# Performance work log

Hardware: AMD Instinct MI355X
Metric: run time of the kernel (lower is better)

The kernel has to match this reference:

```python
import jax, jax.numpy as jnp
import numpy as np

N, D, H, DATT, C, NCLS = 20000, 1024, 512, 256, 10, 4

def setup_inputs() -> dict:
    key = jax.random.key(0)
    ks = jax.random.split(key, 20)
    s = lambda fan_in: 1.0 / np.sqrt(fan_in)
    u = lambda k, shape, fan_in: jax.random.uniform(k, shape, jnp.float32, -s(fan_in), s(fan_in))
    inp = {
        'x': jax.random.normal(ks[0], (N, D), jnp.float32),
        'cluster_id': jax.random.randint(ks[1], (N,), 0, C),
        # per-cluster expert MLP (phi_i): Linear(D,H)+ReLU, Linear(H,H)+ReLU (dropout=identity in eval)
        'W1': u(ks[2], (C, D, H), D), 'b1': u(ks[3], (C, H), D),
        'W2': u(ks[4], (C, H, H), H), 'b2': u(ks[5], (C, H), H),
        # attention_net: Linear(H,H)+ReLU then gated attention (L=H, D=DATT, n_classes=1)
        'fc_W': u(ks[6], (H, H), H), 'fc_b': u(ks[7], (H,), H),
        'Wa': u(ks[8], (H, DATT), H), 'ba': u(ks[9], (DATT,), H),
        'Wb': u(ks[10], (H, DATT), H), 'bb': u(ks[11], (DATT,), H),
        'Wc': u(ks[12], (DATT, 1), DATT), 'bc': u(ks[13], (1,), DATT),
        # rho: Linear(H, DATT)+ReLU
        'rho_W': u(ks[14], (H, DATT), H), 'rho_b': u(ks[15], (DATT,), H),
        # classifier
        'cls_W': u(ks[16], (DATT, NCLS), DATT), 'cls_b': u(ks[17], (NCLS,), DATT),
    }
    return inp

def reference(x, cluster_id, W1, b1, W2, b2, fc_W, fc_b, Wa, ba, Wb, bb, Wc, bc, rho_W, rho_b, cls_W, cls_b):
    # --- per-cluster expert MLPs, vectorized over clusters (no python loop over data) ---
    # h1: [C, N, H] = ReLU(x @ W1_c + b1_c) for every cluster c
    h1 = jax.nn.relu(jnp.einsum('nd,cdh->cnh', x, W1) + b1[:, None, :])
    h2 = jax.nn.relu(jnp.einsum('cnh,chk->cnk', h1, W2) + b2[:, None, :])
    # masked mean-pool per cluster (AdaptiveAvgPool1d(1) over the cluster's tokens)
    mask = (cluster_id[None, :] == jnp.arange(C)[:, None]).astype(h2.dtype)  # [C, N]
    counts = jnp.maximum(mask.sum(axis=1), 1.0)                               # empty cluster -> zeros
    h_cluster = jnp.einsum('cn,cnh->ch', mask, h2) / counts[:, None]          # [C, H]
    # --- attention net: fc + gated attention ---
    h = jax.nn.relu(h_cluster @ fc_W + fc_b)                                  # [C, H]
    a = jnp.tanh(h @ Wa + ba)
    b = jax.nn.sigmoid(h @ Wb + bb)
    A = ((a * b) @ Wc + bc).T                                                 # [1, C]
    A = jax.nn.softmax(A, axis=1)
    h_path = A @ h                                                            # [1, H]
    hr = jax.nn.relu(h_path @ rho_W + rho_b)[0]                               # [DATT] (squeeze)
    logits = (hr @ cls_W + cls_b)[None, :]                                    # [1, NCLS]
    Y_prob = jax.nn.softmax(logits, axis=1)
    Y_hat = jnp.argmax(logits, axis=1, keepdims=True)
    return (logits, Y_prob, Y_hat)
```

## Files before the change

### kernel.cpp

```cpp
#include <hip/hip_runtime.h>
#include <hip/hip_bf16.h>
#include <stdint.h>

#define NT 20000
#define DIM 1024
#define HID 512
#define DATT_N 256
#define NCLUS 10
#define NCLS_N 4
#define NBS 79
#define NRT2 313

typedef __bf16 bf16;
typedef __attribute__((ext_vector_type(8))) __bf16 bf16x8;
typedef __attribute__((ext_vector_type(4))) float f32x4;

__device__ __forceinline__ void gload_lds16(const void* g, void* l) {
  __builtin_amdgcn_global_load_lds(
      (const __attribute__((address_space(1))) unsigned int*)g,
      (__attribute__((address_space(3))) unsigned int*)l, 16, 0, 0);
}


__device__ __forceinline__ void transpose_body(const float* __restrict__ s,
                                               bf16* __restrict__ d, int R, int Cc,
                                               int i0, int j0, float (*t)[33]) {
  int tx = threadIdx.x & 31, ty = threadIdx.x >> 5;
#pragma unroll
  for (int yy = 0; yy < 32; yy += 8)
    t[ty + yy][tx] = s[(size_t)(i0 + ty + yy) * Cc + (j0 + tx)];
  __syncthreads();
#pragma unroll
  for (int yy = 0; yy < 32; yy += 8)
    d[(size_t)(j0 + ty + yy) * R + (i0 + tx)] = (bf16)t[tx][ty + yy];
}

#define ZPB ((NCLUS * HID + 255) / 256)
#define TW1B (16 * 32 * NCLUS)
#define TW2B (16 * 16 * NCLUS)

__global__ __launch_bounds__(256) void setup_kernel(
    const int* __restrict__ cid, int* __restrict__ blkcnt, float* __restrict__ pool,
    const float* __restrict__ W1, bf16* __restrict__ w1t,
    const float* __restrict__ W2, bf16* __restrict__ w2t) {
  __shared__ float t[32][33];
  __shared__ int wcnt[4][16];
  int b = blockIdx.x;
  int tid = threadIdx.x;
  if (b < NBS) {
    int lane = tid & 63, w = tid >> 6;
    int n = b * 256 + tid;
    int mycid = (n < NT) ? cid[n] : -1;
#pragma unroll
    for (int c = 0; c < NCLUS; ++c) {
      unsigned long long m = __ballot(mycid == c);
      if (lane == c) wcnt[w][c] = __popcll(m);
    }
    __syncthreads();
    if (tid < NCLUS)
      blkcnt[b * NCLUS + tid] =
          wcnt[0][tid] + wcnt[1][tid] + wcnt[2][tid] + wcnt[3][tid];
  } else if (b < NBS + ZPB) {
    int i = (b - NBS) * 256 + tid;
    if (i < NCLUS * HID) pool[i] = 0.f;
  } else if (b < NBS + ZPB + TW1B) {
    int bb = b - NBS - ZPB;
    int z = bb >> 9, r = bb & 511, y = r >> 4, x = r & 15;
    transpose_body(W1 + (size_t)z * DIM * HID, w1t + (size_t)z * DIM * HID,
                   DIM, HID, y * 32, x * 32, t);
  } else {
    int bb = b - NBS - ZPB - TW1B;
    int z = bb >> 8, r = bb & 255, y = r >> 4, x = r & 15;
    transpose_body(W2 + (size_t)z * HID * HID, w2t + (size_t)z * HID * HID,
                   HID, HID, y * 32, x * 32, t);
  }
}

__global__ void prefix_kernel(const int* __restrict__ blkcnt, int* __restrict__ blkbase,
                              int* __restrict__ cnt, int* __restrict__ offs) {
  int c = threadIdx.x;
  if (c < NCLUS) {
    int run = 0;
    for (int b = 0; b < NBS; ++b) {
      blkbase[b * NCLUS + c] = run;
      run += blkcnt[b * NCLUS + c];
    }
    cnt[c] = run;
  }
  __syncthreads();
  if (c == 0) {
    int a = 0;
    for (int i = 0; i < NCLUS; ++i) { offs[i] = a; a += cnt[i]; }
    offs[NCLUS] = a;
  }
}

__global__ __launch_bounds__(256) void scatter2_kernel(
    const int* __restrict__ cid, const int* __restrict__ blkbase,
    const int* __restrict__ offs, int* __restrict__ order) {
  __shared__ int wcnt[4][16];
  __shared__ int wbase[4][16];
  int tid = threadIdx.x;
  int lane = tid & 63, w = tid >> 6;
  int n = blockIdx.x * 256 + tid;
  int mycid = (n < NT) ? cid[n] : -1;
  unsigned long long lmask = (lane == 63) ? ~0ull >> 1 : (1ull << lane) - 1;
  int myrank = 0;
#pragma unroll
  for (int c = 0; c < NCLUS; ++c) {
    unsigned long long m = __ballot(mycid == c);
    if (mycid == c) myrank = __popcll(m & lmask);
    if (lane == c) wcnt[w][c] = __popcll(m);
  }
  __syncthreads();
  if (tid < NCLUS) {
    int pre = blkbase[blockIdx.x * NCLUS + tid];
#pragma unroll
    for (int ww = 0; ww < 4; ++ww) { wbase[ww][tid] = pre; pre += wcnt[ww][tid]; }
  }
  __syncthreads();
  if (n < NT) order[offs[mycid] + wbase[w][mycid] + myrank] = n;
}

__global__ void gather_cast(const float* __restrict__ x, const int* __restrict__ order,
                            bf16* __restrict__ xs) {
  int t = blockIdx.x * 256 + threadIdx.x;
  int row = t >> 7;
  if (row >= NT) return;
  int col = (t & 127) << 3;
  const f32x4* p = (const f32x4*)(x + (size_t)order[row] * DIM + col);
  f32x4 u = p[0], v = p[1];
  bf16x8 w;
  w[0] = (bf16)u[0]; w[1] = (bf16)u[1]; w[2] = (bf16)u[2]; w[3] = (bf16)u[3];
  w[4] = (bf16)v[0]; w[5] = (bf16)v[1]; w[6] = (bf16)v[2]; w[7] = (bf16)v[3];
  *(bf16x8*)(xs + (size_t)row * DIM + col) = w;
}

__device__ __forceinline__ bool decode_grp2(int d, int& c, int& rt, int& j) {
  int x8 = d & 7, s = d >> 3;
  int g = (s >> 2) * 8 + x8;
  if (g >= NRT2 * NCLUS) return false;
  j = s & 3;
  c = g / NRT2;
  rt = g - c * NRT2;
  return true;
}


__global__ __launch_bounds__(128, 3) void gemm1_kernel(
    const bf16* __restrict__ xs, const bf16* __restrict__ w1t, const float* __restrict__ b1,
    const int* __restrict__ offs, const int* __restrict__ cnt, bf16* __restrict__ h1) {
  int c, rt, j;
  if (!decode_grp2(blockIdx.x, c, rt, j)) return;
  int cntc = cnt[c];
  int row0 = rt * 64;
  if (row0 >= cntc) return;
  int seg = offs[c];
  int n0 = j * 128;

  __shared__ bf16 Als[64 * 64];
  __shared__ bf16 Bls[128 * 64];

  int tid = threadIdx.x;
  int lane = tid & 63, w = tid >> 6;
  int rx = lane & 7, hi = lane >> 4;

  int kswz = ((lane & 7) ^ (lane >> 3)) << 3;

  const bf16* aptr[4]; int aoff[4];
  const bf16* bptr[8]; int boff[8];
#pragma unroll
  for (int i = 0; i < 4; ++i) {
    int ch = i * 2 + w;
    int r = ch * 8 + (lane >> 3);
    int ar = seg + row0 + r; if (ar > NT - 1) ar = NT - 1;
    aptr[i] = xs + (size_t)ar * DIM + kswz;
    aoff[i] = ch * 512;
  }
#pragma unroll
  for (int i = 0; i < 8; ++i) {
    int ch = i * 2 + w;
    int r = ch * 8 + (lane >> 3);
    bptr[i] = w1t + (size_t)(c * HID + n0 + r) * DIM + kswz;
    boff[i] = ch * 512;
  }

  f32x4 acc[2][8];
#pragma unroll
  for (int m = 0; m < 2; m++)
#pragma unroll
    for (int n = 0; n < 8; n++) acc[m][n] = {0.f, 0.f, 0.f, 0.f};

  for (int k0 = 0; k0 < DIM; k0 += 64) {
#pragma unroll
    for (int i = 0; i < 4; ++i) gload_lds16(aptr[i] + k0, &Als[aoff[i]]);
#pragma unroll
    for (int i = 0; i < 8; ++i) gload_lds16(bptr[i] + k0, &Bls[boff[i]]);
    __syncthreads();
#pragma unroll
    for (int ks = 0; ks < 2; ++ks) {
      int t16 = ks * 4 + hi;
      int ko = ((t16 ^ rx) << 3);
      bf16x8 a[2], b[8];
#pragma unroll
      for (int m = 0; m < 2; m++)
        a[m] = *(const bf16x8*)(&Als[(w * 32 + m * 16 + (lane & 15)) * 64 + ko]);
#pragma unroll
      for (int n = 0; n < 8; n++)
        b[n] = *(const bf16x8*)(&Bls[(n * 16 + (lane & 15)) * 64 + ko]);
#pragma unroll
      for (int m = 0; m < 2; m++)
#pragma unroll
        for (int n = 0; n < 8; n++)
          acc[m][n] = __builtin_amdgcn_mfma_f32_16x16x32_bf16(a[m], b[n], acc[m][n], 0, 0, 0);
    }
    __syncthreads();
  }

  int valid = cntc - row0; if (valid > 64) valid = 64;
#pragma unroll
  for (int n = 0; n < 8; n++) {
    int col = n0 + n * 16 + (lane & 15);
    float bias = b1[c * HID + col];
#pragma unroll
    for (int m = 0; m < 2; m++) {
      int rbase = w * 32 + m * 16 + ((lane >> 4) << 2);
#pragma unroll
      for (int e = 0; e < 4; e++) {
        int r = rbase + e;
        if (r < valid) {
          float v = acc[m][n][e] + bias;
          h1[(size_t)(seg + row0 + r) * HID + col] = (bf16)(v > 0.f ? v : 0.f);
        }
      }
    }
  }
}


__global__ __launch_bounds__(128, 3) void gemm2_kernel(
    const bf16* __restrict__ h1, const bf16* __restrict__ w2t, const float* __restrict__ b2,
    const int* __restrict__ offs, const int* __restrict__ cnt, float* __restrict__ pool) {
  int c, rt, j;
  if (!decode_grp2(blockIdx.x, c, rt, j)) return;
  int cntc = cnt[c];
  int row0 = rt * 64;
  if (row0 >= cntc) return;
  int seg = offs[c];
  int n0 = j * 128;
  int valid = cntc - row0; if (valid > 64) valid = 64;

  __shared__ bf16 Als[64 * 64];
  __shared__ bf16 Bls[128 * 64];

  int tid = threadIdx.x;
  int lane = tid & 63, w = tid >> 6;
  int rx = lane & 7, hi = lane >> 4;
  int kswz = ((lane & 7) ^ (lane >> 3)) << 3;

  const bf16* aptr[4]; int aoff[4];
  const bf16* bptr[8]; int boff[8];
#pragma unroll
  for (int i = 0; i < 4; ++i) {
    int ch = i * 2 + w;
    int r = ch * 8 + (lane >> 3);
    int ar = seg + row0 + r; if (ar > NT - 1) ar = NT - 1;
    aptr[i] = h1 + (size_t)ar * HID + kswz;
    aoff[i] = ch * 512;
  }
#pragma unroll
  for (int i = 0; i < 8; ++i) {
    int ch = i * 2 + w;
    int r = ch * 8 + (lane >> 3);
    bptr[i] = w2t + (size_t)(c * HID + n0 + r) * HID + kswz;
    boff[i] = ch * 512;
  }

  f32x4 acc[2][8];
#pragma unroll
  for (int m = 0; m < 2; m++)
#pragma unroll
    for (int n = 0; n < 8; n++) acc[m][n] = {0.f, 0.f, 0.f, 0.f};

  for (int k0 = 0; k0 < HID; k0 += 64) {
#pragma unroll
    for (int i = 0; i < 4; ++i) gload_lds16(aptr[i] + k0, &Als[aoff[i]]);
#pragma unroll
    for (int i = 0; i < 8; ++i) gload_lds16(bptr[i] + k0, &Bls[boff[i]]);
    __syncthreads();
#pragma unroll
    for (int ks = 0; ks < 2; ++ks) {
      int t16 = ks * 4 + hi;
      int ko = ((t16 ^ rx) << 3);
      bf16x8 a[2], b[8];
#pragma unroll
      for (int m = 0; m < 2; m++)
        a[m] = *(const bf16x8*)(&Als[(w * 32 + m * 16 + (lane & 15)) * 64 + ko]);
#pragma unroll
      for (int n = 0; n < 8; n++)
        b[n] = *(const bf16x8*)(&Bls[(n * 16 + (lane & 15)) * 64 + ko]);
#pragma unroll
      for (int m = 0; m < 2; m++)
#pragma unroll
        for (int n = 0; n < 8; n++)
          acc[m][n] = __builtin_amdgcn_mfma_f32_16x16x32_bf16(a[m], b[n], acc[m][n], 0, 0, 0);
    }
    __syncthreads();
  }

#pragma unroll
  for (int n = 0; n < 8; n++) {
    int col = n0 + n * 16 + (lane & 15);
    float bias = b2[c * HID + col];
    float s = 0.f;
#pragma unroll
    for (int m = 0; m < 2; m++) {
      int rbase = w * 32 + m * 16 + ((lane >> 4) << 2);
#pragma unroll
      for (int e = 0; e < 4; e++) {
        if (rbase + e < valid) {
          float v = acc[m][n][e] + bias;
          s += (v > 0.f ? v : 0.f);
        }
      }
    }
    s += __shfl_xor(s, 16);
    s += __shfl_xor(s, 32);
    if (lane < 16) atomicAdd(&pool[c * HID + col], s);
  }
}


__global__ __launch_bounds__(256) void tail_fc(
    const float* __restrict__ pool, const int* __restrict__ cnt,
    const float* __restrict__ fcW, const float* __restrict__ fcb,
    float* __restrict__ hbuf) {
  int c = blockIdx.x >> 3;
  int jt = blockIdx.x & 7;
  __shared__ float hc[HID];
  __shared__ float red[4][64];
  int tid = threadIdx.x;
  float inv = 1.f / fmaxf((float)cnt[c], 1.f);
  for (int k = tid; k < HID; k += 256) hc[k] = pool[c * HID + k] * inv;
  __syncthreads();
  int jl = tid & 63, kg = tid >> 6;
  int j = jt * 64 + jl;
  float s = 0.f;
#pragma unroll 4
  for (int k = kg * 128; k < kg * 128 + 128; ++k) s += hc[k] * fcW[(size_t)k * HID + j];
  red[kg][jl] = s;
  __syncthreads();
  if (kg == 0) {
    float v = red[0][jl] + red[1][jl] + red[2][jl] + red[3][jl] + fcb[j];
    hbuf[c * HID + j] = fmaxf(v, 0.f);
  }
}

__global__ __launch_bounds__(1024) void tail_att(
    const float* __restrict__ hbuf,
    const float* __restrict__ Wa, const float* __restrict__ ba,
    const float* __restrict__ Wb, const float* __restrict__ bb,
    const float* __restrict__ Wc, const float* __restrict__ bc,
    float* __restrict__ score) {
  int c = blockIdx.x;
  __shared__ float h[HID];
  __shared__ float ra[4][DATT_N];
  __shared__ float rb[4][DATT_N];
  __shared__ float sc[DATT_N];
  int tid = threadIdx.x;
  for (int k = tid; k < HID; k += 1024) h[k] = hbuf[c * HID + k];
  __syncthreads();
  int jl = tid & 255, kg = tid >> 8;
  float sa = 0.f, sb = 0.f;
#pragma unroll 4
  for (int k = kg * 128; k < kg * 128 + 128; ++k) {
    float hv = h[k];
    sa += hv * Wa[(size_t)k * DATT_N + jl];
    sb += hv * Wb[(size_t)k * DATT_N + jl];
  }
  ra[kg][jl] = sa;
  rb[kg][jl] = sb;
  __syncthreads();
  if (kg == 0) {
    float va = ra[0][jl] + ra[1][jl] + ra[2][jl] + ra[3][jl] + ba[jl];
    float vb = rb[0][jl] + rb[1][jl] + rb[2][jl] + rb[3][jl] + bb[jl];
    float av = tanhf(va);
    float bv = 1.f / (1.f + expf(-vb));
    sc[jl] = av * bv * Wc[jl];
  }
  __syncthreads();
  for (int s2 = 128; s2 > 0; s2 >>= 1) {
    if (tid < s2) sc[tid] += sc[tid + s2];
    __syncthreads();
  }
  if (tid == 0) score[c] = sc[0] + bc[0];
}

__global__ __launch_bounds__(1024) void tail_fin(
    const float* __restrict__ score, const float* __restrict__ hbuf,
    const float* __restrict__ rhoW, const float* __restrict__ rhob,
    const float* __restrict__ clsW, const float* __restrict__ clsb,
    float* __restrict__ out) {
  __shared__ float Asm[NCLUS];
  __shared__ float hp[HID];
  __shared__ float rr[4][DATT_N];
  __shared__ float hr[DATT_N];
  __shared__ float lg[NCLS_N];
  int tid = threadIdx.x;
  if (tid == 0) {
    float mx = -1e30f;
    for (int c = 0; c < NCLUS; c++) mx = fmaxf(mx, score[c]);
    float sum = 0.f, e[NCLUS];
    for (int c = 0; c < NCLUS; c++) { e[c] = expf(score[c] - mx); sum += e[c]; }
    for (int c = 0; c < NCLUS; c++) Asm[c] = e[c] / sum;
  }
  __syncthreads();
  if (tid < HID) {
    float s = 0.f;
#pragma unroll
    for (int c = 0; c < NCLUS; c++) s += Asm[c] * hbuf[c * HID + tid];
    hp[tid] = s;
  }
  __syncthreads();
  int jl = tid & 255, kg = tid >> 8;
  float s = 0.f;
#pragma unroll 4
  for (int k = kg * 128; k < kg * 128 + 128; ++k) s += hp[k] * rhoW[(size_t)k * DATT_N + jl];
  rr[kg][jl] = s;
  __syncthreads();
  if (kg == 0) hr[jl] = fmaxf(rr[0][jl] + rr[1][jl] + rr[2][jl] + rr[3][jl] + rhob[jl], 0.f);
  __syncthreads();
  if (tid < NCLS_N * 64) {
    int t = tid >> 6, l = tid & 63;
    float cs = 0.f;
    for (int j = l; j < DATT_N; j += 64) cs += hr[j] * clsW[j * NCLS_N + t];
#pragma unroll
    for (int w = 32; w > 0; w >>= 1) cs += __shfl_xor(cs, w);
    if (l == 0) lg[t] = cs + clsb[t];
  }
  __syncthreads();
  if (tid == 0) {
    float mx = lg[0];
    int am = 0;
    for (int t = 1; t < NCLS_N; t++) if (lg[t] > mx) { mx = lg[t]; am = t; }
    float sum = 0.f, e[NCLS_N];
    for (int t = 0; t < NCLS_N; t++) { e[t] = expf(lg[t] - mx); sum += e[t]; }
    for (int t = 0; t < NCLS_N; t++) {
      out[t] = lg[t];
      out[NCLS_N + t] = e[t] / sum;
    }
    out[2 * NCLS_N] = (float)am;
  }
}


extern "C" void kernel_launch(void* const* d_in, const int* in_sizes, int n_in,
                              void* d_out, int out_size, void* d_ws, size_t ws_size,
                              hipStream_t stream) {
  const float* x    = (const float*)d_in[0];
  const int*   cid  = (const int*)d_in[1];
  const float* W1   = (const float*)d_in[2];
  const float* b1   = (const float*)d_in[3];
  const float* W2   = (const float*)d_in[4];
  const float* b2   = (const float*)d_in[5];
  const float* fcW  = (const float*)d_in[6];
  const float* fcb  = (const float*)d_in[7];
  const float* Wa   = (const float*)d_in[8];
  const float* ba   = (const float*)d_in[9];
  const float* Wb   = (const float*)d_in[10];
  const float* bb   = (const float*)d_in[11];
  const float* Wc   = (const float*)d_in[12];
  const float* bc   = (const float*)d_in[13];
  const float* rhoW = (const float*)d_in[14];
  const float* rhob = (const float*)d_in[15];
  const float* clsW = (const float*)d_in[16];
  const float* clsb = (const float*)d_in[17];
  float* out = (float*)d_out;

  char* ws = (char*)d_ws;
  int*   cnt     = (int*)(ws + 0);
  int*   offs    = (int*)(ws + 64);
  float* score   = (float*)(ws + 128);
  int*   blkcnt  = (int*)(ws + 256);
  int*   blkbase = (int*)(ws + 256 + 4096);
  int*   order   = (int*)(ws + 256 + 8192);
  float* pool    = (float*)(ws + 256 + 8192 + 80000);
  float* hbuf    = (float*)(ws + 256 + 8192 + 80000 + NCLUS * HID * 4);
  size_t o = 256 + 8192 + 80000 + 2ull * NCLUS * HID * 4;
  o = (o + 255) & ~(size_t)255;
  bf16* w1t = (bf16*)(ws + o); o += (size_t)NCLUS * HID * DIM * 2;
  bf16* w2t = (bf16*)(ws + o); o += (size_t)NCLUS * HID * HID * 2;
  bf16* h1  = (bf16*)(ws + o); o += (size_t)NT * HID * 2;
  bf16* xs  = (bf16*)(ws + o); o += (size_t)NT * DIM * 2;

  setup_kernel<<<dim3(NBS + ZPB + TW1B + TW2B), dim3(256), 0, stream>>>(
      cid, blkcnt, pool, W1, w1t, W2, w2t);
  prefix_kernel<<<dim3(1), dim3(64), 0, stream>>>(blkcnt, blkbase, cnt, offs);
  scatter2_kernel<<<dim3(NBS), dim3(256), 0, stream>>>(cid, blkbase, offs, order);
  gather_cast<<<dim3(NT * 128 / 256), dim3(256), 0, stream>>>(x, order, xs);

  int nblk = 8 * ((NRT2 * NCLUS + 7) / 8) * 4;
  gemm1_kernel<<<dim3(nblk), dim3(128), 0, stream>>>(xs, w1t, b1, offs, cnt, h1);
  gemm2_kernel<<<dim3(nblk), dim3(128), 0, stream>>>(h1, w2t, b2, offs, cnt, pool);

  tail_fc<<<dim3(NCLUS * 8), dim3(256), 0, stream>>>(pool, cnt, fcW, fcb, hbuf);
  tail_att<<<dim3(NCLUS), dim3(1024), 0, stream>>>(hbuf, Wa, ba, Wb, bb, Wc, bc, score);
  tail_fin<<<dim3(1), dim3(1024), 0, stream>>>(score, hbuf, rhoW, rhob, clsW, clsb, out);
}
```

Baseline: 137.1 us.

## Merge prefix into scatter, fuse gather with weight transposes, fuse tail fc+attention

Result: slower. 151.6 us (+10.5%).

```diff
diff --git a/kernel.cpp b/kernel.cpp
--- a/kernel.cpp
+++ b/kernel.cpp
@@ -10,6 +10,7 @@
 #define NCLS_N 4
 #define NBS 79
 #define NRT2 313
+#define GB 10000
 
 typedef __bf16 bf16;
 typedef __attribute__((ext_vector_type(8))) __bf16 bf16x8;
@@ -22,28 +23,10 @@
 }
 
 
-__device__ __forceinline__ void transpose_body(const float* __restrict__ s,
-                                               bf16* __restrict__ d, int R, int Cc,
-                                               int i0, int j0, float (*t)[33]) {
-  int tx = threadIdx.x & 31, ty = threadIdx.x >> 5;
-#pragma unroll
-  for (int yy = 0; yy < 32; yy += 8)
-    t[ty + yy][tx] = s[(size_t)(i0 + ty + yy) * Cc + (j0 + tx)];
-  __syncthreads();
-#pragma unroll
-  for (int yy = 0; yy < 32; yy += 8)
-    d[(size_t)(j0 + ty + yy) * R + (i0 + tx)] = (bf16)t[tx][ty + yy];
-}
-
 #define ZPB ((NCLUS * HID + 255) / 256)
-#define TW1B (16 * 32 * NCLUS)
-#define TW2B (16 * 16 * NCLUS)
-
-__global__ __launch_bounds__(256) void setup_kernel(
-    const int* __restrict__ cid, int* __restrict__ blkcnt, float* __restrict__ pool,
-    const float* __restrict__ W1, bf16* __restrict__ w1t,
-    const float* __restrict__ W2, bf16* __restrict__ w2t) {
-  __shared__ float t[32][33];
+
+__global__ __launch_bounds__(256) void hist_zero_kernel(
+    const int* __restrict__ cid, int* __restrict__ blkcnt, float* __restrict__ pool) {
   __shared__ int wcnt[4][16];
   int b = blockIdx.x;
   int tid = threadIdx.x;
@@ -60,49 +43,46 @@
     if (tid < NCLUS)
       blkcnt[b * NCLUS + tid] =
           wcnt[0][tid] + wcnt[1][tid] + wcnt[2][tid] + wcnt[3][tid];
-  } else if (b < NBS + ZPB) {
+  } else {
     int i = (b - NBS) * 256 + tid;
     if (i < NCLUS * HID) pool[i] = 0.f;
-  } else if (b < NBS + ZPB + TW1B) {
-    int bb = b - NBS - ZPB;
-    int z = bb >> 9, r = bb & 511, y = r >> 4, x = r & 15;
-    transpose_body(W1 + (size_t)z * DIM * HID, w1t + (size_t)z * DIM * HID,
-                   DIM, HID, y * 32, x * 32, t);
-  } else {
-    int bb = b - NBS - ZPB - TW1B;
-    int z = bb >> 8, r = bb & 255, y = r >> 4, x = r & 15;
-    transpose_body(W2 + (size_t)z * HID * HID, w2t + (size_t)z * HID * HID,
-                   HID, HID, y * 32, x * 32, t);
-  }
-}
-
-__global__ void prefix_kernel(const int* __restrict__ blkcnt, int* __restrict__ blkbase,
-                              int* __restrict__ cnt, int* __restrict__ offs) {
-  int c = threadIdx.x;
-  if (c < NCLUS) {
-    int run = 0;
-    for (int b = 0; b < NBS; ++b) {
-      blkbase[b * NCLUS + c] = run;
-      run += blkcnt[b * NCLUS + c];
-    }
-    cnt[c] = run;
-  }
-  __syncthreads();
-  if (c == 0) {
-    int a = 0;
-    for (int i = 0; i < NCLUS; ++i) { offs[i] = a; a += cnt[i]; }
-    offs[NCLUS] = a;
-  }
-}
-
-__global__ __launch_bounds__(256) void scatter2_kernel(
-    const int* __restrict__ cid, const int* __restrict__ blkbase,
-    const int* __restrict__ offs, int* __restrict__ order) {
+  }
+}
+
+
+__global__ __launch_bounds__(256) void scatter_kernel(
+    const int* __restrict__ cid, const int* __restrict__ blkcnt,
+    int* __restrict__ cnt, int* __restrict__ offs, int* __restrict__ order) {
+  __shared__ int sbase[16];
+  __shared__ int scnt[16];
+  __shared__ int soffs[16];
   __shared__ int wcnt[4][16];
   __shared__ int wbase[4][16];
   int tid = threadIdx.x;
   int lane = tid & 63, w = tid >> 6;
-  int n = blockIdx.x * 256 + tid;
+  int bx = blockIdx.x;
+  if (tid < NCLUS) {
+    int base = 0, run = 0;
+    for (int b = 0; b < NBS; ++b) {
+      int v = blkcnt[b * NCLUS + tid];
+      if (b < bx) base += v;
+      run += v;
+    }
+    sbase[tid] = base;
+    scnt[tid] = run;
+  }
+  __syncthreads();
+  if (tid == 0) {
+    int a = 0;
+    for (int i = 0; i < NCLUS; ++i) { soffs[i] = a; a += scnt[i]; }
+    soffs[NCLUS] = a;
+  }
+  __syncthreads();
+  if (bx == 0 && tid <= NCLUS) {
+    if (tid < NCLUS) cnt[tid] = scnt[tid];
+    offs[tid] = soffs[tid];
+  }
+  int n = bx * 256 + tid;
   int mycid = (n < NT) ? cid[n] : -1;
   unsigned long long lmask = (lane == 63) ? ~0ull >> 1 : (1ull << lane) - 1;
   int myrank = 0;
@@ -114,26 +94,59 @@
   }
   __syncthreads();
   if (tid < NCLUS) {
-    int pre = blkbase[blockIdx.x * NCLUS + tid];
+    int pre = sbase[tid];
 #pragma unroll
     for (int ww = 0; ww < 4; ++ww) { wbase[ww][tid] = pre; pre += wcnt[ww][tid]; }
   }
   __syncthreads();
-  if (n < NT) order[offs[mycid] + wbase[w][mycid] + myrank] = n;
-}
-
-__global__ void gather_cast(const float* __restrict__ x, const int* __restrict__ order,
-                            bf16* __restrict__ xs) {
-  int t = blockIdx.x * 256 + threadIdx.x;
-  int row = t >> 7;
-  if (row >= NT) return;
-  int col = (t & 127) << 3;
-  const f32x4* p = (const f32x4*)(x + (size_t)order[row] * DIM + col);
-  f32x4 u = p[0], v = p[1];
-  bf16x8 w;
-  w[0] = (bf16)u[0]; w[1] = (bf16)u[1]; w[2] = (bf16)u[2]; w[3] = (bf16)u[3];
-  w[4] = (bf16)v[0]; w[5] = (bf16)v[1]; w[6] = (bf16)v[2]; w[7] = (bf16)v[3];
-  *(bf16x8*)(xs + (size_t)row * DIM + col) = w;
+  if (n < NT) order[soffs[mycid] + wbase[w][mycid] + myrank] = n;
+}
+
+
+__device__ __forceinline__ void transpose_body(const float* __restrict__ s,
+                                               bf16* __restrict__ d, int R, int Cc,
+                                               int i0, int j0, float (*t)[33]) {
+  int tx = threadIdx.x & 31, ty = threadIdx.x >> 5;
+#pragma unroll
+  for (int yy = 0; yy < 32; yy += 8)
+    t[ty + yy][tx] = s[(size_t)(i0 + ty + yy) * Cc + (j0 + tx)];
+  __syncthreads();
+#pragma unroll
+  for (int yy = 0; yy < 32; yy += 8)
+    d[(size_t)(j0 + ty + yy) * R + (i0 + tx)] = (bf16)t[tx][ty + yy];
+}
+
+#define TW1B (16 * 32 * NCLUS)
+#define TW2B (16 * 16 * NCLUS)
+
+__global__ __launch_bounds__(256) void gather_tr_kernel(
+    const float* __restrict__ x, const int* __restrict__ order, bf16* __restrict__ xs,
+    const float* __restrict__ W1, bf16* __restrict__ w1t,
+    const float* __restrict__ W2, bf16* __restrict__ w2t) {
+  __shared__ float t[32][33];
+  int b = blockIdx.x;
+  if (b < GB) {
+    int tt = b * 256 + threadIdx.x;
+    int row = tt >> 7;
+    if (row >= NT) return;
+    int col = (tt & 127) << 3;
+    const f32x4* p = (const f32x4*)(x + (size_t)order[row] * DIM + col);
+    f32x4 u = p[0], v = p[1];
+    bf16x8 w;
+    w[0] = (bf16)u[0]; w[1] = (bf16)u[1]; w[2] = (bf16)u[2]; w[3] = (bf16)u[3];
+    w[4] = (bf16)v[0]; w[5] = (bf16)v[1]; w[6] = (bf16)v[2]; w[7] = (bf16)v[3];
+    *(bf16x8*)(xs + (size_t)row * DIM + col) = w;
+  } else if (b < GB + TW1B) {
+    int bb = b - GB;
+    int z = bb >> 9, r = bb & 511, y = r >> 4, xq = r & 15;
+    transpose_body(W1 + (size_t)z * DIM * HID, w1t + (size_t)z * DIM * HID,
+                   DIM, HID, y * 32, xq * 32, t);
+  } else {
+    int bb = b - GB - TW1B;
+    int z = bb >> 8, r = bb & 255, y = r >> 4, xq = r & 15;
+    transpose_body(W2 + (size_t)z * HID * HID, w2t + (size_t)z * HID * HID,
+                   HID, HID, y * 32, xq * 32, t);
+  }
 }
 
 __device__ __forceinline__ bool decode_grp2(int d, int& c, int& rt, int& j) {
@@ -164,7 +177,6 @@
   int tid = threadIdx.x;
   int lane = tid & 63, w = tid >> 6;
   int rx = lane & 7, hi = lane >> 4;
-
   int kswz = ((lane & 7) ^ (lane >> 3)) << 3;
 
   const bf16* aptr[4]; int aoff[4];
@@ -331,62 +343,57 @@
 }
 
 
-__global__ __launch_bounds__(256) void tail_fc(
+__global__ __launch_bounds__(1024) void tail_fca(
     const float* __restrict__ pool, const int* __restrict__ cnt,
     const float* __restrict__ fcW, const float* __restrict__ fcb,
-    float* __restrict__ hbuf) {
-  int c = blockIdx.x >> 3;
-  int jt = blockIdx.x & 7;
-  __shared__ float hc[HID];
-  __shared__ float red[4][64];
-  int tid = threadIdx.x;
-  float inv = 1.f / fmaxf((float)cnt[c], 1.f);
-  for (int k = tid; k < HID; k += 256) hc[k] = pool[c * HID + k] * inv;
-  __syncthreads();
-  int jl = tid & 63, kg = tid >> 6;
-  int j = jt * 64 + jl;
-  float s = 0.f;
-#pragma unroll 4
-  for (int k = kg * 128; k < kg * 128 + 128; ++k) s += hc[k] * fcW[(size_t)k * HID + j];
-  red[kg][jl] = s;
-  __syncthreads();
-  if (kg == 0) {
-    float v = red[0][jl] + red[1][jl] + red[2][jl] + red[3][jl] + fcb[j];
-    hbuf[c * HID + j] = fmaxf(v, 0.f);
-  }
-}
-
-__global__ __launch_bounds__(1024) void tail_att(
-    const float* __restrict__ hbuf,
     const float* __restrict__ Wa, const float* __restrict__ ba,
     const float* __restrict__ Wb, const float* __restrict__ bb,
     const float* __restrict__ Wc, const float* __restrict__ bc,
-    float* __restrict__ score) {
+    float* __restrict__ hbuf, float* __restrict__ score) {
   int c = blockIdx.x;
+  __shared__ float hc[HID];
   __shared__ float h[HID];
+  __shared__ float red[2][HID];
   __shared__ float ra[4][DATT_N];
   __shared__ float rb[4][DATT_N];
   __shared__ float sc[DATT_N];
   int tid = threadIdx.x;
-  for (int k = tid; k < HID; k += 1024) h[k] = hbuf[c * HID + k];
-  __syncthreads();
-  int jl = tid & 255, kg = tid >> 8;
-  float sa = 0.f, sb = 0.f;
+  float inv = 1.f / fmaxf((float)cnt[c], 1.f);
+  for (int k = tid; k < HID; k += 1024) hc[k] = pool[c * HID + k] * inv;
+  __syncthreads();
+  {
+    int j = tid & 511, kg = tid >> 9;
+    float s = 0.f;
 #pragma unroll 4
-  for (int k = kg * 128; k < kg * 128 + 128; ++k) {
-    float hv = h[k];
-    sa += hv * Wa[(size_t)k * DATT_N + jl];
-    sb += hv * Wb[(size_t)k * DATT_N + jl];
-  }
-  ra[kg][jl] = sa;
-  rb[kg][jl] = sb;
-  __syncthreads();
-  if (kg == 0) {
-    float va = ra[0][jl] + ra[1][jl] + ra[2][jl] + ra[3][jl] + ba[jl];
-    float vb = rb[0][jl] + rb[1][jl] + rb[2][jl] + rb[3][jl] + bb[jl];
+    for (int k = kg * 256; k < kg * 256 + 256; ++k) s += hc[k] * fcW[(size_t)k * HID + j];
+    red[kg][j] = s;
+  }
+  __syncthreads();
+  if (tid < HID) {
+    float v = fmaxf(red[0][tid] + red[1][tid] + fcb[tid], 0.f);
+    h[tid] = v;
+    hbuf[c * HID + tid] = v;
+  }
+  __syncthreads();
+  {
+    int jl = tid & 255, kg = tid >> 8;
+    float sa = 0.f, sb = 0.f;
+#pragma unroll 4
+    for (int k = kg * 128; k < kg * 128 + 128; ++k) {
+      float hv = h[k];
+      sa += hv * Wa[(size_t)k * DATT_N + jl];
+      sb += hv * Wb[(size_t)k * DATT_N + jl];
+    }
+    ra[kg][jl] = sa;
+    rb[kg][jl] = sb;
+  }
+  __syncthreads();
+  if (tid < DATT_N) {
+    float va = ra[0][tid] + ra[1][tid] + ra[2][tid] + ra[3][tid] + ba[tid];
+    float vb = rb[0][tid] + rb[1][tid] + rb[2][tid] + rb[3][tid] + bb[tid];
     float av = tanhf(va);
     float bv = 1.f / (1.f + expf(-vb));
-    sc[jl] = av * bv * Wc[jl];
+    sc[tid] = av * bv * Wc[tid];
   }
   __syncthreads();
   for (int s2 = 128; s2 > 0; s2 >>= 1) {
@@ -395,6 +402,7 @@
   }
   if (tid == 0) score[c] = sc[0] + bc[0];
 }
+
 
 __global__ __launch_bounds__(1024) void tail_fin(
     const float* __restrict__ score, const float* __restrict__ hbuf,
@@ -482,28 +490,26 @@
   int*   offs    = (int*)(ws + 64);
   float* score   = (float*)(ws + 128);
   int*   blkcnt  = (int*)(ws + 256);
-  int*   blkbase = (int*)(ws + 256 + 4096);
-  int*   order   = (int*)(ws + 256 + 8192);
-  float* pool    = (float*)(ws + 256 + 8192 + 80000);
-  float* hbuf    = (float*)(ws + 256 + 8192 + 80000 + NCLUS * HID * 4);
-  size_t o = 256 + 8192 + 80000 + 2ull * NCLUS * HID * 4;
+  int*   order   = (int*)(ws + 256 + 4096);
+  float* pool    = (float*)(ws + 256 + 4096 + 80000);
+  float* hbuf    = (float*)(ws + 256 + 4096 + 80000 + NCLUS * HID * 4);
+  size_t o = 256 + 4096 + 80000 + 2ull * NCLUS * HID * 4;
   o = (o + 255) & ~(size_t)255;
   bf16* w1t = (bf16*)(ws + o); o += (size_t)NCLUS * HID * DIM * 2;
   bf16* w2t = (bf16*)(ws + o); o += (size_t)NCLUS * HID * HID * 2;
   bf16* h1  = (bf16*)(ws + o); o += (size_t)NT * HID * 2;
   bf16* xs  = (bf16*)(ws + o); o += (size_t)NT * DIM * 2;
 
-  setup_kernel<<<dim3(NBS + ZPB + TW1B + TW2B), dim3(256), 0, stream>>>(
-      cid, blkcnt, pool, W1, w1t, W2, w2t);
-  prefix_kernel<<<dim3(1), dim3(64), 0, stream>>>(blkcnt, blkbase, cnt, offs);
-  scatter2_kernel<<<dim3(NBS), dim3(256), 0, stream>>>(cid, blkbase, offs, order);
-  gather_cast<<<dim3(NT * 128 / 256), dim3(256), 0, stream>>>(x, order, xs);
+  hist_zero_kernel<<<dim3(NBS + ZPB), dim3(256), 0, stream>>>(cid, blkcnt, pool);
+  scatter_kernel<<<dim3(NBS), dim3(256), 0, stream>>>(cid, blkcnt, cnt, offs, order);
+  gather_tr_kernel<<<dim3(GB + TW1B + TW2B), dim3(256), 0, stream>>>(
+      x, order, xs, W1, w1t, W2, w2t);
 
   int nblk = 8 * ((NRT2 * NCLUS + 7) / 8) * 4;
   gemm1_kernel<<<dim3(nblk), dim3(128), 0, stream>>>(xs, w1t, b1, offs, cnt, h1);
   gemm2_kernel<<<dim3(nblk), dim3(128), 0, stream>>>(h1, w2t, b2, offs, cnt, pool);
 
-  tail_fc<<<dim3(NCLUS * 8), dim3(256), 0, stream>>>(pool, cnt, fcW, fcb, hbuf);
-  tail_att<<<dim3(NCLUS), dim3(1024), 0, stream>>>(hbuf, Wa, ba, Wb, bb, Wc, bc, score);
+  tail_fca<<<dim3(NCLUS), dim3(1024), 0, stream>>>(pool, cnt, fcW, fcb, Wa, ba, Wb, bb,
+                                                   Wc, bc, hbuf, score);
   tail_fin<<<dim3(1), dim3(1024), 0, stream>>>(score, hbuf, rhoW, rhob, clsW, clsb, out);
 }
```

## Fuse gather-cast into GEMM1, merge prefix into scatter, vectorize weight transpose

Applied to the files above, without the earlier changes.

After: 137.5 us. Within noise of the previous version (+0.3%).

```diff
diff --git a/kernel.cpp b/kernel.cpp
--- a/kernel.cpp
+++ b/kernel.cpp
@@ -22,28 +22,32 @@
 }
 
 
-__device__ __forceinline__ void transpose_body(const float* __restrict__ s,
-                                               bf16* __restrict__ d, int R, int Cc,
-                                               int i0, int j0, float (*t)[33]) {
-  int tx = threadIdx.x & 31, ty = threadIdx.x >> 5;
+#define ZPB 20
+#define TW1B (32 * 4 * NCLUS)
+#define TW2B (16 * 4 * NCLUS)
+
+__device__ __forceinline__ void tr_body(const float* __restrict__ s, bf16* __restrict__ d,
+                                        int R, int Cc, int i0, int j0, float (*t)[128]) {
+  int tid = threadIdx.x;
+  int cr = tid >> 5;
+  int cc4 = (tid & 31) << 2;
 #pragma unroll
   for (int yy = 0; yy < 32; yy += 8)
-    t[ty + yy][tx] = s[(size_t)(i0 + ty + yy) * Cc + (j0 + tx)];
-  __syncthreads();
-#pragma unroll
-  for (int yy = 0; yy < 32; yy += 8)
-    d[(size_t)(j0 + ty + yy) * R + (i0 + tx)] = (bf16)t[tx][ty + yy];
-}
-
-#define ZPB ((NCLUS * HID + 255) / 256)
-#define TW1B (16 * 32 * NCLUS)
-#define TW2B (16 * 16 * NCLUS)
+    *(f32x4*)&t[yy + cr][cc4] = *(const f32x4*)&s[(size_t)(i0 + yy + cr) * Cc + j0 + cc4];
+  __syncthreads();
+  int col = tid >> 1, h = (tid & 1) << 4;
+  bf16 tmp[16];
+#pragma unroll
+  for (int k = 0; k < 16; ++k) tmp[k] = (bf16)t[h + k][col];
+  *(bf16x8*)&d[(size_t)(j0 + col) * R + i0 + h] = *(bf16x8*)&tmp[0];
+  *(bf16x8*)&d[(size_t)(j0 + col) * R + i0 + h + 8] = *(bf16x8*)&tmp[8];
+}
 
 __global__ __launch_bounds__(256) void setup_kernel(
     const int* __restrict__ cid, int* __restrict__ blkcnt, float* __restrict__ pool,
     const float* __restrict__ W1, bf16* __restrict__ w1t,
     const float* __restrict__ W2, bf16* __restrict__ w2t) {
-  __shared__ float t[32][33];
+  __shared__ float t[32][128];
   __shared__ int wcnt[4][16];
   int b = blockIdx.x;
   int tid = threadIdx.x;
@@ -65,44 +69,51 @@
     if (i < NCLUS * HID) pool[i] = 0.f;
   } else if (b < NBS + ZPB + TW1B) {
     int bb = b - NBS - ZPB;
-    int z = bb >> 9, r = bb & 511, y = r >> 4, x = r & 15;
-    transpose_body(W1 + (size_t)z * DIM * HID, w1t + (size_t)z * DIM * HID,
-                   DIM, HID, y * 32, x * 32, t);
+    int z = bb >> 7, r = bb & 127, rt = r >> 2, ct = r & 3;
+    tr_body(W1 + (size_t)z * DIM * HID, w1t + (size_t)z * DIM * HID,
+            DIM, HID, rt * 32, ct * 128, t);
   } else {
     int bb = b - NBS - ZPB - TW1B;
-    int z = bb >> 8, r = bb & 255, y = r >> 4, x = r & 15;
-    transpose_body(W2 + (size_t)z * HID * HID, w2t + (size_t)z * HID * HID,
-                   HID, HID, y * 32, x * 32, t);
-  }
-}
-
-__global__ void prefix_kernel(const int* __restrict__ blkcnt, int* __restrict__ blkbase,
-                              int* __restrict__ cnt, int* __restrict__ offs) {
-  int c = threadIdx.x;
-  if (c < NCLUS) {
-    int run = 0;
-    for (int b = 0; b < NBS; ++b) {
-      blkbase[b * NCLUS + c] = run;
-      run += blkcnt[b * NCLUS + c];
-    }
-    cnt[c] = run;
-  }
-  __syncthreads();
-  if (c == 0) {
-    int a = 0;
-    for (int i = 0; i < NCLUS; ++i) { offs[i] = a; a += cnt[i]; }
-    offs[NCLUS] = a;
-  }
-}
-
-__global__ __launch_bounds__(256) void scatter2_kernel(
-    const int* __restrict__ cid, const int* __restrict__ blkbase,
-    const int* __restrict__ offs, int* __restrict__ order) {
+    int z = bb >> 6, r = bb & 63, rt = r >> 2, ct = r & 3;
+    tr_body(W2 + (size_t)z * HID * HID, w2t + (size_t)z * HID * HID,
+            HID, HID, rt * 32, ct * 128, t);
+  }
+}
+
+
+__global__ __launch_bounds__(256) void scatter_kernel(
+    const int* __restrict__ cid, const int* __restrict__ blkcnt,
+    int* __restrict__ cnt, int* __restrict__ offs, int* __restrict__ order) {
+  __shared__ int sbase[16];
+  __shared__ int scnt[16];
+  __shared__ int soffs[16];
   __shared__ int wcnt[4][16];
   __shared__ int wbase[4][16];
   int tid = threadIdx.x;
   int lane = tid & 63, w = tid >> 6;
-  int n = blockIdx.x * 256 + tid;
+  int bx = blockIdx.x;
+  if (tid < NCLUS) {
+    int base = 0, run = 0;
+    for (int b = 0; b < NBS; ++b) {
+      int v = blkcnt[b * NCLUS + tid];
+      if (b < bx) base += v;
+      run += v;
+    }
+    sbase[tid] = base;
+    scnt[tid] = run;
+  }
+  __syncthreads();
+  if (tid == 0) {
+    int a = 0;
+    for (int i = 0; i < NCLUS; ++i) { soffs[i] = a; a += scnt[i]; }
+    soffs[NCLUS] = a;
+  }
+  __syncthreads();
+  if (bx == 0 && tid <= NCLUS) {
+    if (tid < NCLUS) cnt[tid] = scnt[tid];
+    offs[tid] = soffs[tid];
+  }
+  int n = bx * 256 + tid;
   int mycid = (n < NT) ? cid[n] : -1;
   unsigned long long lmask = (lane == 63) ? ~0ull >> 1 : (1ull << lane) - 1;
   int myrank = 0;
@@ -114,26 +125,12 @@
   }
   __syncthreads();
   if (tid < NCLUS) {
-    int pre = blkbase[blockIdx.x * NCLUS + tid];
+    int pre = sbase[tid];
 #pragma unroll
     for (int ww = 0; ww < 4; ++ww) { wbase[ww][tid] = pre; pre += wcnt[ww][tid]; }
   }
   __syncthreads();
-  if (n < NT) order[offs[mycid] + wbase[w][mycid] + myrank] = n;
-}
-
-__global__ void gather_cast(const float* __restrict__ x, const int* __restrict__ order,
-                            bf16* __restrict__ xs) {
-  int t = blockIdx.x * 256 + threadIdx.x;
-  int row = t >> 7;
-  if (row >= NT) return;
-  int col = (t & 127) << 3;
-  const f32x4* p = (const f32x4*)(x + (size_t)order[row] * DIM + col);
-  f32x4 u = p[0], v = p[1];
-  bf16x8 w;
-  w[0] = (bf16)u[0]; w[1] = (bf16)u[1]; w[2] = (bf16)u[2]; w[3] = (bf16)u[3];
-  w[4] = (bf16)v[0]; w[5] = (bf16)v[1]; w[6] = (bf16)v[2]; w[7] = (bf16)v[3];
-  *(bf16x8*)(xs + (size_t)row * DIM + col) = w;
+  if (n < NT) order[soffs[mycid] + wbase[w][mycid] + myrank] = n;
 }
 
 __device__ __forceinline__ bool decode_grp2(int d, int& c, int& rt, int& j) {
@@ -147,8 +144,9 @@
 }
 
 
-__global__ __launch_bounds__(128, 3) void gemm1_kernel(
-    const bf16* __restrict__ xs, const bf16* __restrict__ w1t, const float* __restrict__ b1,
+__global__ __launch_bounds__(128, 2) void gemm1_kernel(
+    const float* __restrict__ x, const int* __restrict__ order,
+    const bf16* __restrict__ w1t, const float* __restrict__ b1,
     const int* __restrict__ offs, const int* __restrict__ cnt, bf16* __restrict__ h1) {
   int c, rt, j;
   if (!decode_grp2(blockIdx.x, c, rt, j)) return;
@@ -158,25 +156,22 @@
   int seg = offs[c];
   int n0 = j * 128;
 
-  __shared__ bf16 Als[64 * 64];
+  __shared__ float Af[64 * 64];
   __shared__ bf16 Bls[128 * 64];
+  __shared__ int s_ord[64];
 
   int tid = threadIdx.x;
   int lane = tid & 63, w = tid >> 6;
+  if (tid < 64) {
+    int ar = seg + row0 + tid; if (ar > NT - 1) ar = NT - 1;
+    s_ord[tid] = order[ar];
+  }
+  __syncthreads();
+
   int rx = lane & 7, hi = lane >> 4;
-
   int kswz = ((lane & 7) ^ (lane >> 3)) << 3;
 
-  const bf16* aptr[4]; int aoff[4];
   const bf16* bptr[8]; int boff[8];
-#pragma unroll
-  for (int i = 0; i < 4; ++i) {
-    int ch = i * 2 + w;
-    int r = ch * 8 + (lane >> 3);
-    int ar = seg + row0 + r; if (ar > NT - 1) ar = NT - 1;
-    aptr[i] = xs + (size_t)ar * DIM + kswz;
-    aoff[i] = ch * 512;
-  }
 #pragma unroll
   for (int i = 0; i < 8; ++i) {
     int ch = i * 2 + w;
@@ -184,6 +179,16 @@
     bptr[i] = w1t + (size_t)(c * HID + n0 + r) * DIM + kswz;
     boff[i] = ch * 512;
   }
+  const float* fptr[8]; int foff[8];
+#pragma unroll
+  for (int i = 0; i < 8; ++i) {
+    int ch = i * 2 + w;
+    int r = ch * 4 + (lane >> 4);
+    int j16 = lane & 15;
+    int colf = ((((j16 >> 1) ^ (r & 7)) << 1) | (j16 & 1)) << 2;
+    fptr[i] = x + (size_t)s_ord[r] * DIM + colf;
+    foff[i] = ch * 256;
+  }
 
   f32x4 acc[2][8];
 #pragma unroll
@@ -193,21 +198,29 @@
 
   for (int k0 = 0; k0 < DIM; k0 += 64) {
 #pragma unroll
-    for (int i = 0; i < 4; ++i) gload_lds16(aptr[i] + k0, &Als[aoff[i]]);
+    for (int i = 0; i < 8; ++i) gload_lds16(fptr[i] + k0, &Af[foff[i]]);
 #pragma unroll
     for (int i = 0; i < 8; ++i) gload_lds16(bptr[i] + k0, &Bls[boff[i]]);
     __syncthreads();
 #pragma unroll
     for (int ks = 0; ks < 2; ++ks) {
-      int t16 = ks * 4 + hi;
-      int ko = ((t16 ^ rx) << 3);
+      int pp = ks * 4 + hi;
+      int kof = ((pp ^ rx) << 3);
+      int kob = ((pp ^ rx) << 3);
       bf16x8 a[2], b[8];
 #pragma unroll
-      for (int m = 0; m < 2; m++)
-        a[m] = *(const bf16x8*)(&Als[(w * 32 + m * 16 + (lane & 15)) * 64 + ko]);
+      for (int m = 0; m < 2; m++) {
+        int rr = w * 32 + m * 16 + (lane & 15);
+        const f32x4* ap = (const f32x4*)&Af[rr * 64 + kof];
+        f32x4 u = ap[0], v = ap[1];
+        bf16x8 t;
+        t[0] = (bf16)u[0]; t[1] = (bf16)u[1]; t[2] = (bf16)u[2]; t[3] = (bf16)u[3];
+        t[4] = (bf16)v[0]; t[5] = (bf16)v[1]; t[6] = (bf16)v[2]; t[7] = (bf16)v[3];
+        a[m] = t;
+      }
 #pragma unroll
       for (int n = 0; n < 8; n++)
-        b[n] = *(const bf16x8*)(&Bls[(n * 16 + (lane & 15)) * 64 + ko]);
+        b[n] = *(const bf16x8*)(&Bls[(n * 16 + (lane & 15)) * 64 + kob]);
 #pragma unroll
       for (int m = 0; m < 2; m++)
 #pragma unroll
@@ -482,25 +495,21 @@
   int*   offs    = (int*)(ws + 64);
   float* score   = (float*)(ws + 128);
   int*   blkcnt  = (int*)(ws + 256);
-  int*   blkbase = (int*)(ws + 256 + 4096);
-  int*   order   = (int*)(ws + 256 + 8192);
-  float* pool    = (float*)(ws + 256 + 8192 + 80000);
-  float* hbuf    = (float*)(ws + 256 + 8192 + 80000 + NCLUS * HID * 4);
-  size_t o = 256 + 8192 + 80000 + 2ull * NCLUS * HID * 4;
+  int*   order   = (int*)(ws + 256 + 4096);
+  float* pool    = (float*)(ws + 256 + 4096 + 80000);
+  float* hbuf    = (float*)(ws + 256 + 4096 + 80000 + NCLUS * HID * 4);
+  size_t o = 256 + 4096 + 80000 + 2ull * NCLUS * HID * 4;
   o = (o + 255) & ~(size_t)255;
   bf16* w1t = (bf16*)(ws + o); o += (size_t)NCLUS * HID * DIM * 2;
   bf16* w2t = (bf16*)(ws + o); o += (size_t)NCLUS * HID * HID * 2;
   bf16* h1  = (bf16*)(ws + o); o += (size_t)NT * HID * 2;
-  bf16* xs  = (bf16*)(ws + o); o += (size_t)NT * DIM * 2;
 
   setup_kernel<<<dim3(NBS + ZPB + TW1B + TW2B), dim3(256), 0, stream>>>(
       cid, blkcnt, pool, W1, w1t, W2, w2t);
-  prefix_kernel<<<dim3(1), dim3(64), 0, stream>>>(blkcnt, blkbase, cnt, offs);
-  scatter2_kernel<<<dim3(NBS), dim3(256), 0, stream>>>(cid, blkbase, offs, order);
-  gather_cast<<<dim3(NT * 128 / 256), dim3(256), 0, stream>>>(x, order, xs);
+  scatter_kernel<<<dim3(NBS), dim3(256), 0, stream>>>(cid, blkcnt, cnt, offs, order);
 
   int nblk = 8 * ((NRT2 * NCLUS + 7) / 8) * 4;
-  gemm1_kernel<<<dim3(nblk), dim3(128), 0, stream>>>(xs, w1t, b1, offs, cnt, h1);
+  gemm1_kernel<<<dim3(nblk), dim3(128), 0, stream>>>(x, order, w1t, b1, offs, cnt, h1);
   gemm2_kernel<<<dim3(nblk), dim3(128), 0, stream>>>(h1, w2t, b2, offs, cnt, pool);
 
   tail_fc<<<dim3(NCLUS * 8), dim3(256), 0, stream>>>(pool, cnt, fcW, fcb, hbuf);
```
